# Kernel optimization log

Measured on AMD Instinct MI355X. Metric: run time of the kernel, lower is better.

The kernel has to match this reference:

```python
import jax, jax.numpy as jnp
import numpy as np

N_HEADS, D_MODEL, D_HEAD = 16, 1024, 64
INIT_RANGE = 0.02
BATCH, SEQ = 4, 2048


def setup_inputs() -> dict:
    key = jax.random.key(0)
    k0, k1, k2, k3, k4 = jax.random.split(key, 5)
    resid = jax.random.normal(k0, (BATCH, SEQ, D_MODEL), dtype=jnp.float32)
    w_q = INIT_RANGE * jax.random.normal(k1, (N_HEADS, D_MODEL, D_HEAD), dtype=jnp.float32)
    w_k = INIT_RANGE * jax.random.normal(k2, (N_HEADS, D_MODEL, D_HEAD), dtype=jnp.float32)
    w_v = INIT_RANGE * jax.random.normal(k3, (N_HEADS, D_MODEL, D_HEAD), dtype=jnp.float32)
    w_o = INIT_RANGE * jax.random.normal(k4, (N_HEADS, D_HEAD, D_MODEL), dtype=jnp.float32)
    return {"resid": resid, "w_q": w_q, "w_k": w_k, "w_v": w_v, "w_o": w_o}


def reference(resid, w_q, w_k, w_v, w_o):
    # resid: [b, s, m]; w_q/k/v: [h, m, d]; w_o: [h, d, m]
    qs = jnp.einsum('bsm,hmd->bhsd', resid, w_q)
    ks = jnp.einsum('bsm,hmd->bhsd', resid, w_k)
    vs = jnp.einsum('bsm,hmd->bhsd', resid, w_v)
    attn = jnp.einsum('bhqd,bhkd->bhqk', qs, ks)  # full O(n^2) scores
    s = attn.shape[-1]
    causal = jnp.tril(jnp.ones((s, s), dtype=bool))  # True = keep
    attn = jnp.where(causal, attn, -jnp.inf)
    attn = jax.nn.softmax(attn / jnp.sqrt(jnp.float32(D_HEAD)), axis=-1)
    z = jnp.einsum('bhqk,bhkd->bhqd', attn, vs)
    out = jnp.einsum('bhsd,hdm->bsm', z, w_o)
    return out
```

## Files before the change

### kernel.cpp

```cpp
#include <hip/hip_runtime.h>


typedef __attribute__((ext_vector_type(8))) short short8;
typedef __attribute__((ext_vector_type(4))) float f32x4;
typedef __attribute__((ext_vector_type(16))) float f32x16;

#define GLDS16(g, l) __builtin_amdgcn_global_load_lds(                        \
    (const __attribute__((address_space(1))) unsigned int*)(g),               \
    (__attribute__((address_space(3))) unsigned int*)(l), 16, 0, 0)

static __device__ __forceinline__ unsigned short f2b(float f) {
  union { float f; unsigned u; } c; c.f = f;
  unsigned r = c.u + 0x7fffu + ((c.u >> 16) & 1u);
  return (unsigned short)(r >> 16);
}

__global__ void k_cast(const float* __restrict__ x, unsigned short* __restrict__ o, int n4) {
  int i = blockIdx.x * blockDim.x + threadIdx.x;
  if (i >= n4) return;
  float4 v = reinterpret_cast<const float4*>(x)[i];
  ushort4 u;
  u.x = f2b(v.x); u.y = f2b(v.y); u.z = f2b(v.z); u.w = f2b(v.w);
  reinterpret_cast<ushort4*>(o)[i] = u;
}

__global__ void k_trans_qkv(const float* __restrict__ wq, const float* __restrict__ wk,
                            const float* __restrict__ wv, unsigned short* __restrict__ o) {
  __shared__ float t[64][65];
  int blk = blockIdx.x;
  int mt = blk & 15;
  int h = (blk >> 4) & 15;
  int which = blk >> 8;
  const float* w = which == 0 ? wq : (which == 1 ? wk : wv);
  int tid = threadIdx.x;
  int m0 = mt * 64;
  #pragma unroll
  for (int rep = 0; rep < 16; ++rep) {
    int idx = rep * 256 + tid;
    int r = idx >> 6, c = idx & 63;
    t[r][c] = w[(h * 1024 + m0 + r) * 64 + c];
  }
  __syncthreads();
  #pragma unroll
  for (int rep = 0; rep < 16; ++rep) {
    int idx = rep * 256 + tid;
    int dr = idx >> 6, mc = idx & 63;
    o[(which * 1024 + h * 64 + dr) * 1024 + m0 + mc] = f2b(t[mc][dr]);
  }
}

__global__ void k_trans_wo(const float* __restrict__ wo, unsigned short* __restrict__ o) {
  __shared__ float t[64][65];
  int blk = blockIdx.x;
  int mt = blk & 15, kt = blk >> 4;
  int tid = threadIdx.x;
  int k0 = kt * 64, m0 = mt * 64;
  #pragma unroll
  for (int rep = 0; rep < 16; ++rep) {
    int idx = rep * 256 + tid;
    int r = idx >> 6, c = idx & 63;
    t[r][c] = wo[(k0 + r) * 1024 + m0 + c];
  }
  __syncthreads();
  #pragma unroll
  for (int rep = 0; rep < 16; ++rep) {
    int idx = rep * 256 + tid;
    int r = idx >> 6, c = idx & 63;
    o[(m0 + r) * 1024 + k0 + c] = f2b(t[c][r]);
  }
}

__global__ __launch_bounds__(256) void k_gemm_qkv(const unsigned short* __restrict__ A,
                                                  const unsigned short* __restrict__ Bt,
                                                  unsigned short* __restrict__ Qb,
                                                  unsigned short* __restrict__ Kc,
                                                  unsigned short* __restrict__ Vc) {
  __shared__ unsigned short As[128 * 32];
  __shared__ unsigned short Bs[128 * 32];
  const int bm = blockIdx.x, bn = blockIdx.y;
  const int tid = threadIdx.x;
  const int lane = tid & 63, wid = tid >> 6;
  const int wr = wid >> 1, wc = wid & 1;
  const int fr = lane & 15, fq = lane >> 4;
  const int which = bn >> 3;

  f32x4 acc[4][4];
  #pragma unroll
  for (int i = 0; i < 4; ++i)
    #pragma unroll
    for (int n = 0; n < 4; ++n) acc[i][n] = f32x4{0.f, 0.f, 0.f, 0.f};

  const int arow = tid >> 2, acol = (tid & 3) * 8;
  const int lds0 = tid * 8, lds1 = (tid + 256) * 8;
  const unsigned short* aG0 = A + (bm * 128 + arow) * 1024 + acol;
  const unsigned short* aG1 = A + (bm * 128 + arow + 64) * 1024 + acol;
  const unsigned short* bG0 = Bt + (bn * 128 + arow) * 1024 + acol;
  const unsigned short* bG1 = Bt + (bn * 128 + arow + 64) * 1024 + acol;

  const unsigned short* Ar = As + (wr * 64 + fr) * 32 + fq * 8;
  const unsigned short* Br = Bs + (wc * 64 + fr) * 32 + fq * 8;

  if (which == 2) {
    for (int k0 = 0; k0 < 1024; k0 += 32) {
      __syncthreads();
      GLDS16(aG0 + k0, As + lds0);
      GLDS16(aG1 + k0, As + lds1);
      GLDS16(bG0 + k0, Bs + lds0);
      GLDS16(bG1 + k0, Bs + lds1);
      asm volatile("s_waitcnt vmcnt(0)" ::: "memory");
      __syncthreads();
      short8 a[4], b[4];
      #pragma unroll
      for (int i = 0; i < 4; ++i) a[i] = *reinterpret_cast<const short8*>(Ar + i * 512);
      #pragma unroll
      for (int n = 0; n < 4; ++n) b[n] = *reinterpret_cast<const short8*>(Br + n * 512);
      #pragma unroll
      for (int i = 0; i < 4; ++i)
        #pragma unroll
        for (int n = 0; n < 4; ++n)
          acc[i][n] = __builtin_amdgcn_mfma_f32_16x16x32_bf16(a[i], b[n], acc[i][n], 0, 0, 0);
    }
    const int colb = bn * 128 + wc * 64 + fr - 2048;
    const int rowb = bm * 128 + wr * 64 + fq * 4;
    #pragma unroll
    for (int n = 0; n < 4; ++n) {
      const int rc = colb + n * 16;
      const int h = rc >> 6, d = rc & 63;
      #pragma unroll
      for (int i = 0; i < 4; ++i) {
        const int row = rowb + i * 16;
        const int b_ = row >> 11, s = row & 2047;
        const int bh = b_ * 16 + h;
        const int c = s >> 5, kk = s & 31;
        const int r = d >> 1;
        const int sl = (((d & 1) * 4 + (kk >> 3)) ^ (r & 7));
        ushort4 v;
        v.x = f2b(acc[i][n][0]); v.y = f2b(acc[i][n][1]);
        v.z = f2b(acc[i][n][2]); v.w = f2b(acc[i][n][3]);
        *reinterpret_cast<ushort4*>(
            &Vc[((size_t)(bh * 64 + c)) * 2048 + r * 64 + sl * 8 + (kk & 7)]) = v;
      }
    }
  } else {
    for (int k0 = 0; k0 < 1024; k0 += 32) {
      __syncthreads();
      GLDS16(aG0 + k0, As + lds0);
      GLDS16(aG1 + k0, As + lds1);
      GLDS16(bG0 + k0, Bs + lds0);
      GLDS16(bG1 + k0, Bs + lds1);
      asm volatile("s_waitcnt vmcnt(0)" ::: "memory");
      __syncthreads();
      short8 a[4], b[4];
      #pragma unroll
      for (int i = 0; i < 4; ++i) a[i] = *reinterpret_cast<const short8*>(Ar + i * 512);
      #pragma unroll
      for (int n = 0; n < 4; ++n) b[n] = *reinterpret_cast<const short8*>(Br + n * 512);
      #pragma unroll
      for (int i = 0; i < 4; ++i)
        #pragma unroll
        for (int n = 0; n < 4; ++n)
          acc[i][n] = __builtin_amdgcn_mfma_f32_16x16x32_bf16(b[n], a[i], acc[i][n], 0, 0, 0);
    }
    const float CS = 0.125f * 1.44269504088896340736f;
    const int rowS = bm * 128 + wr * 64 + fr;
    const int cold = bn * 128 + wc * 64 + fq * 4;
    #pragma unroll
    for (int i = 0; i < 4; ++i) {
      const int S = rowS + i * 16;
      const int b_ = S >> 11, s = S & 2047;
      #pragma unroll
      for (int n = 0; n < 4; ++n) {
        const int col = cold + n * 16;
        const int rc = col & 1023;
        const int h = rc >> 6, d0 = rc & 63;
        const int bh = b_ * 16 + h;
        if (which == 0) {
          ushort4 u;
          u.x = f2b(acc[i][n][0] * CS); u.y = f2b(acc[i][n][1] * CS);
          u.z = f2b(acc[i][n][2] * CS); u.w = f2b(acc[i][n][3] * CS);
          *reinterpret_cast<ushort4*>(&Qb[((size_t)bh * 2048 + s) * 64 + d0]) = u;
        } else {
          const int c = s >> 5, r = s & 31;
          const int dsw0 = (((d0 >> 3) ^ (r & 7)) << 3) | (d0 & 7);
          ushort4 u;
          u.x = f2b(acc[i][n][0]); u.y = f2b(acc[i][n][1]);
          u.z = f2b(acc[i][n][2]); u.w = f2b(acc[i][n][3]);
          *reinterpret_cast<ushort4*>(
              &Kc[(((size_t)(bh * 64 + c)) * 32 + r) * 64 + dsw0]) = u;
        }
      }
    }
  }
}


static __device__ __forceinline__ f32x16 mfma32(short8 a, short8 b, f32x16 c) {
  return __builtin_amdgcn_mfma_f32_32x32x16_bf16(a, b, c, 0, 0, 0);
}

template<bool MASKED>
static __device__ __forceinline__ void compute_chunk(
    const unsigned short* __restrict__ Kl, const unsigned short* __restrict__ Vl,
    int q, int hi,
    const short8& Qf0, const short8& Qf1, const short8& Qf2, const short8& Qf3,
    f32x16& accA, f32x16& accB, float& lsum) {
  const int qs = q & 7;
  const short8 kf0 = *reinterpret_cast<const short8*>(Kl + q * 64 + (((0 + hi) ^ qs) << 3));
  const short8 kf1 = *reinterpret_cast<const short8*>(Kl + q * 64 + (((2 + hi) ^ qs) << 3));
  const short8 kf2 = *reinterpret_cast<const short8*>(Kl + q * 64 + (((4 + hi) ^ qs) << 3));
  const short8 kf3 = *reinterpret_cast<const short8*>(Kl + q * 64 + (((6 + hi) ^ qs) << 3));
  const int vr = q >> 1, vs = (q & 1) * 4, vw = vr & 7;
  const short8 v00 = *reinterpret_cast<const short8*>(Vl + vr * 64 + (((vs + hi) ^ vw) << 3));
  const short8 v01 = *reinterpret_cast<const short8*>(Vl + vr * 64 + (((vs + 2 + hi) ^ vw) << 3));
  const short8 v10 = *reinterpret_cast<const short8*>(Vl + (vr + 16) * 64 + (((vs + hi) ^ vw) << 3));
  const short8 v11 = *reinterpret_cast<const short8*>(Vl + (vr + 16) * 64 + (((vs + 2 + hi) ^ vw) << 3));

  f32x16 s = {0.f,0.f,0.f,0.f,0.f,0.f,0.f,0.f,0.f,0.f,0.f,0.f,0.f,0.f,0.f,0.f};
  s = mfma32(kf0, Qf0, s);
  s = mfma32(kf1, Qf1, s);
  s = mfma32(kf2, Qf2, s);
  s = mfma32(kf3, Qf3, s);

  float p[16];
  #pragma unroll
  for (int r = 0; r < 16; ++r) {
    if (MASKED) {
      const int kr = (r & 3) + 8 * (r >> 2) + 4 * hi;
      p[r] = (kr <= q) ? __builtin_amdgcn_exp2f(s[r]) : 0.f;
    } else {
      p[r] = __builtin_amdgcn_exp2f(s[r]);
    }
  }
  float t0 = (p[0] + p[1]) + (p[2] + p[3]);
  float t1 = (p[4] + p[5]) + (p[6] + p[7]);
  float t2 = (p[8] + p[9]) + (p[10] + p[11]);
  float t3 = (p[12] + p[13]) + (p[14] + p[15]);
  lsum += (t0 + t1) + (t2 + t3);

  unsigned W[8], X[8];
  #pragma unroll
  for (int i = 0; i < 8; ++i)
    asm("v_cvt_pk_bf16_f32 %0, %1, %2" : "=v"(W[i]) : "v"(p[2 * i]), "v"(p[2 * i + 1]));
  #pragma unroll
  for (int i = 0; i < 8; ++i) X[i] = __shfl_xor(W[i], 32);

  union { unsigned u[4]; short8 v; } fa0, fa1;
  fa0.u[0] = hi ? X[2] : W[0];
  fa0.u[1] = hi ? X[3] : W[1];
  fa0.u[2] = hi ? W[2] : X[0];
  fa0.u[3] = hi ? W[3] : X[1];
  fa1.u[0] = hi ? X[6] : W[4];
  fa1.u[1] = hi ? X[7] : W[5];
  fa1.u[2] = hi ? W[6] : X[4];
  fa1.u[3] = hi ? W[7] : X[5];

  accA = mfma32(fa0.v, v00, accA);
  accA = mfma32(fa1.v, v01, accA);
  accB = mfma32(fa0.v, v10, accB);
  accB = mfma32(fa1.v, v11, accB);
}

static __device__ __forceinline__ void store_tile(unsigned short* __restrict__ Zb,
    int b_, int h, int q0, int q, int hi,
    const f32x16& a0, const f32x16& a1, float lsum) {
  const float lt = lsum + __shfl_xor(lsum, 32);
  const float rl = 1.f / lt;
  #pragma unroll
  for (int r = 0; r < 16; ++r) {
    const int qr = (r & 3) + 8 * (r >> 2) + 4 * hi;
    const float rlr = __shfl(rl, qr);
    unsigned short* dst = Zb + ((size_t)(b_ * 2048 + q0 + qr)) * 1024 + h * 64 + q;
    dst[0]  = f2b(a0[r] * rlr);
    dst[32] = f2b(a1[r] * rlr);
  }
}

__global__ __launch_bounds__(256, 2) void k_attn(const unsigned short* __restrict__ Qb,
                                                 const unsigned short* __restrict__ Kc,
                                                 const unsigned short* __restrict__ Vc,
                                                 unsigned short* __restrict__ Zb) {
  __shared__ __align__(16) unsigned short Kbuf[2][2048];
  __shared__ __align__(16) unsigned short Vbuf[2][2048];
  const int tid = threadIdx.x;
  const int lane = tid & 63, w = tid >> 6;
  const int q = lane & 31, hi = lane >> 5;
  const int bid = blockIdx.x;
  const int bh = (bid & 7) * 8 + ((bid >> 3) & 7);
  const int P1 = bid >> 6;
  const int b_ = bh >> 4, h = bh & 15;

  const unsigned short* Qbh = Qb + (size_t)bh * 2048 * 64;
  const unsigned short* Kch = Kc + (size_t)bh * 64 * 2048;
  const unsigned short* Vch = Vc + (size_t)bh * 64 * 2048;

  #pragma unroll 1
  for (int t = 0; t < 2; ++t) {
    const int P = t ? (15 - P1) : P1;
    const int q0 = 128 * P + 32 * w;
    const int cmax = 4 * P + w;
    const int C = 4 * P + 4;

    const unsigned short* Qp = Qbh + (size_t)(q0 + q) * 64 + hi * 8;
    const short8 Qf0 = *reinterpret_cast<const short8*>(Qp);
    const short8 Qf1 = *reinterpret_cast<const short8*>(Qp + 16);
    const short8 Qf2 = *reinterpret_cast<const short8*>(Qp + 32);
    const short8 Qf3 = *reinterpret_cast<const short8*>(Qp + 48);

    f32x16 a0 = {0.f,0.f,0.f,0.f,0.f,0.f,0.f,0.f,0.f,0.f,0.f,0.f,0.f,0.f,0.f,0.f};
    f32x16 a1 = a0;
    float l = 0.f;

    GLDS16(Kch + tid * 8, &Kbuf[0][tid * 8]);
    GLDS16(Vch + tid * 8, &Vbuf[0][tid * 8]);

    for (int c = 0; c < C; ++c) {
      if (c + 1 < C) {
        const int par = (c + 1) & 1;
        GLDS16(Kch + (size_t)(c + 1) * 2048 + tid * 8, &Kbuf[par][tid * 8]);
        GLDS16(Vch + (size_t)(c + 1) * 2048 + tid * 8, &Vbuf[par][tid * 8]);
        asm volatile("s_waitcnt vmcnt(2)" ::: "memory");
      } else {
        asm volatile("s_waitcnt vmcnt(0)" ::: "memory");
      }
      __syncthreads();
      if (c <= cmax) {
        const int par = c & 1;
        if (c == cmax)
          compute_chunk<true>(Kbuf[par], Vbuf[par], q, hi, Qf0, Qf1, Qf2, Qf3, a0, a1, l);
        else
          compute_chunk<false>(Kbuf[par], Vbuf[par], q, hi, Qf0, Qf1, Qf2, Qf3, a0, a1, l);
      }
      __syncthreads();
    }
    store_tile(Zb, b_, h, q0, q, hi, a0, a1, l);
  }
}

__global__ __launch_bounds__(256) void k_gemm_out(const unsigned short* __restrict__ A,
                                                  const unsigned short* __restrict__ Bt,
                                                  float* __restrict__ Out) {
  __shared__ unsigned short As[128 * 32];
  __shared__ unsigned short Bs[128 * 32];
  const int bm = blockIdx.x, bn = blockIdx.y;
  const int tid = threadIdx.x;
  const int lane = tid & 63, wid = tid >> 6;
  const int wr = wid >> 1, wc = wid & 1;
  const int fr = lane & 15, fq = lane >> 4;

  f32x4 acc[4][4];
  #pragma unroll
  for (int i = 0; i < 4; ++i)
    #pragma unroll
    for (int n = 0; n < 4; ++n) acc[i][n] = f32x4{0.f, 0.f, 0.f, 0.f};

  const int arow = tid >> 2, acol = (tid & 3) * 8;
  const int lds0 = tid * 8, lds1 = (tid + 256) * 8;
  const unsigned short* aG0 = A + (bm * 128 + arow) * 1024 + acol;
  const unsigned short* aG1 = A + (bm * 128 + arow + 64) * 1024 + acol;
  const unsigned short* bG0 = Bt + (bn * 128 + arow) * 1024 + acol;
  const unsigned short* bG1 = Bt + (bn * 128 + arow + 64) * 1024 + acol;

  const unsigned short* Ar = As + (wr * 64 + fr) * 32 + fq * 8;
  const unsigned short* Br = Bs + (wc * 64 + fr) * 32 + fq * 8;

  for (int k0 = 0; k0 < 1024; k0 += 32) {
    __syncthreads();
    GLDS16(aG0 + k0, As + lds0);
    GLDS16(aG1 + k0, As + lds1);
    GLDS16(bG0 + k0, Bs + lds0);
    GLDS16(bG1 + k0, Bs + lds1);
    asm volatile("s_waitcnt vmcnt(0)" ::: "memory");
    __syncthreads();
    short8 a[4], b[4];
    #pragma unroll
    for (int i = 0; i < 4; ++i) a[i] = *reinterpret_cast<const short8*>(Ar + i * 512);
    #pragma unroll
    for (int n = 0; n < 4; ++n) b[n] = *reinterpret_cast<const short8*>(Br + n * 512);
    #pragma unroll
    for (int i = 0; i < 4; ++i)
      #pragma unroll
      for (int n = 0; n < 4; ++n)
        acc[i][n] = __builtin_amdgcn_mfma_f32_16x16x32_bf16(b[n], a[i], acc[i][n], 0, 0, 0);
  }

  const int rowS = bm * 128 + wr * 64 + fr;
  const int cold = bn * 128 + wc * 64 + fq * 4;
  #pragma unroll
  for (int i = 0; i < 4; ++i) {
    const int S = rowS + i * 16;
    #pragma unroll
    for (int n = 0; n < 4; ++n) {
      const int m0 = cold + n * 16;
      float4 v;
      v.x = acc[i][n][0]; v.y = acc[i][n][1]; v.z = acc[i][n][2]; v.w = acc[i][n][3];
      *reinterpret_cast<float4*>(&Out[(size_t)S * 1024 + m0]) = v;
    }
  }
}

extern "C" void kernel_launch(void* const* d_in, const int* in_sizes, int n_in,
                              void* d_out, int out_size, void* d_ws, size_t ws_size,
                              hipStream_t stream) {
  const float* resid = (const float*)d_in[0];
  const float* w_q = (const float*)d_in[1];
  const float* w_k = (const float*)d_in[2];
  const float* w_v = (const float*)d_in[3];
  const float* w_o = (const float*)d_in[4];
  float* out = (float*)d_out;

  char* ws = (char*)d_ws;
  const size_t MB = 1u << 20;
  unsigned short* Xb = (unsigned short*)(ws);
  unsigned short* W3 = (unsigned short*)(ws + 16 * MB);
  unsigned short* Wo = (unsigned short*)(ws + 22 * MB);
  unsigned short* Qb = (unsigned short*)(ws + 24 * MB);
  unsigned short* Kc = (unsigned short*)(ws + 40 * MB);
  unsigned short* Vc = (unsigned short*)(ws + 56 * MB);
  unsigned short* Zb = Xb;

  hipLaunchKernelGGL(k_cast, dim3(8192), dim3(256), 0, stream, resid, Xb, 8192 * 1024 / 4);
  hipLaunchKernelGGL(k_trans_qkv, dim3(768), dim3(256), 0, stream, w_q, w_k, w_v, W3);
  hipLaunchKernelGGL(k_trans_wo, dim3(256), dim3(256), 0, stream, w_o, Wo);
  hipLaunchKernelGGL(k_gemm_qkv, dim3(64, 24), dim3(256), 0, stream, Xb, W3, Qb, Kc, Vc);
  hipLaunchKernelGGL(k_attn, dim3(512), dim3(256), 0, stream, Qb, Kc, Vc, Zb);
  hipLaunchKernelGGL(k_gemm_out, dim3(64, 8), dim3(256), 0, stream, Zb, Wo, out);
}
```

Before: 189.3 us.

## Double-buffer GEMM LDS tiles and pre-swizzle bf16 operands against bank conflicts

The QKV and output-projection GEMMs now double-buffer their LDS tiles, so the global-to-LDS load of the next K slice is issued before the MFMAs on the current one. This drops one barrier per iteration and overlaps memory with compute. All bf16 operand producers (the cast, the weight transposes and the attention output store) now write a swizzled layout within each 32-column group. The GEMMs read LDS with the matching XOR slot, which avoids LDS bank conflicts without changing the direct global_load_lds copy. LDS per block doubles, which may reduce occupancy, and every producer and consumer must agree on the swizzle.

```diff
diff --git a/kernel.cpp b/kernel.cpp
--- a/kernel.cpp
+++ b/kernel.cpp
@@ -13,6 +13,10 @@
   union { float f; unsigned u; } c; c.f = f;
   unsigned r = c.u + 0x7fffu + ((c.u >> 16) & 1u);
   return (unsigned short)(r >> 16);
+}
+
+static __device__ __forceinline__ int swzc(int row, int c) {
+  return (c & ~31) | ((((c >> 3) & 3) ^ ((row >> 1) & 3)) << 3) | (c & 7);
 }
 
 __global__ void k_cast(const float* __restrict__ x, unsigned short* __restrict__ o, int n4) {
@@ -21,7 +25,9 @@
   float4 v = reinterpret_cast<const float4*>(x)[i];
   ushort4 u;
   u.x = f2b(v.x); u.y = f2b(v.y); u.z = f2b(v.z); u.w = f2b(v.w);
-  reinterpret_cast<ushort4*>(o)[i] = u;
+  const int flat = i * 4;
+  const int row = flat >> 10, c = flat & 1023;
+  *reinterpret_cast<ushort4*>(&o[row * 1024 + swzc(row, c)]) = u;
 }
 
 __global__ void k_trans_qkv(const float* __restrict__ wq, const float* __restrict__ wk,
@@ -45,7 +51,8 @@
   for (int rep = 0; rep < 16; ++rep) {
     int idx = rep * 256 + tid;
     int dr = idx >> 6, mc = idx & 63;
-    o[(which * 1024 + h * 64 + dr) * 1024 + m0 + mc] = f2b(t[mc][dr]);
+    const int row = which * 1024 + h * 64 + dr;
+    o[row * 1024 + swzc(dr, m0 + mc)] = f2b(t[mc][dr]);
   }
 }
 
@@ -66,7 +73,7 @@
   for (int rep = 0; rep < 16; ++rep) {
     int idx = rep * 256 + tid;
     int r = idx >> 6, c = idx & 63;
-    o[(m0 + r) * 1024 + k0 + c] = f2b(t[c][r]);
+    o[(m0 + r) * 1024 + swzc(r, k0 + c)] = f2b(t[c][r]);
   }
 }
 
@@ -75,8 +82,8 @@
                                                   unsigned short* __restrict__ Qb,
                                                   unsigned short* __restrict__ Kc,
                                                   unsigned short* __restrict__ Vc) {
-  __shared__ unsigned short As[128 * 32];
-  __shared__ unsigned short Bs[128 * 32];
+  __shared__ unsigned short As[2][128 * 32];
+  __shared__ unsigned short Bs[2][128 * 32];
   const int bm = blockIdx.x, bn = blockIdx.y;
   const int tid = threadIdx.x;
   const int lane = tid & 63, wid = tid >> 6;
@@ -91,35 +98,56 @@
     for (int n = 0; n < 4; ++n) acc[i][n] = f32x4{0.f, 0.f, 0.f, 0.f};
 
   const int arow = tid >> 2, acol = (tid & 3) * 8;
-  const int lds0 = tid * 8, lds1 = (tid + 256) * 8;
+  const int lds0 = tid * 8, lds1 = tid * 8 + 2048;
   const unsigned short* aG0 = A + (bm * 128 + arow) * 1024 + acol;
   const unsigned short* aG1 = A + (bm * 128 + arow + 64) * 1024 + acol;
   const unsigned short* bG0 = Bt + (bn * 128 + arow) * 1024 + acol;
   const unsigned short* bG1 = Bt + (bn * 128 + arow + 64) * 1024 + acol;
 
-  const unsigned short* Ar = As + (wr * 64 + fr) * 32 + fq * 8;
-  const unsigned short* Br = Bs + (wc * 64 + fr) * 32 + fq * 8;
-
-  if (which == 2) {
-    for (int k0 = 0; k0 < 1024; k0 += 32) {
-      __syncthreads();
-      GLDS16(aG0 + k0, As + lds0);
-      GLDS16(aG1 + k0, As + lds1);
-      GLDS16(bG0 + k0, Bs + lds0);
-      GLDS16(bG1 + k0, Bs + lds1);
-      asm volatile("s_waitcnt vmcnt(0)" ::: "memory");
-      __syncthreads();
-      short8 a[4], b[4];
-      #pragma unroll
-      for (int i = 0; i < 4; ++i) a[i] = *reinterpret_cast<const short8*>(Ar + i * 512);
-      #pragma unroll
-      for (int n = 0; n < 4; ++n) b[n] = *reinterpret_cast<const short8*>(Br + n * 512);
+  const int rowA = (wr * 64 + fr) * 32;
+  const int rowB = (wc * 64 + fr) * 32;
+  const int slot = ((fq ^ ((fr >> 1) & 3)) << 3);
+
+  GLDS16(aG0, As[0] + lds0);
+  GLDS16(aG1, As[0] + lds1);
+  GLDS16(bG0, Bs[0] + lds0);
+  GLDS16(bG1, Bs[0] + lds1);
+  asm volatile("s_waitcnt vmcnt(0)" ::: "memory");
+  __syncthreads();
+
+  for (int k0 = 0; k0 < 1024; k0 += 32) {
+    const int cur = (k0 >> 5) & 1;
+    if (k0 + 32 < 1024) {
+      GLDS16(aG0 + k0 + 32, As[cur ^ 1] + lds0);
+      GLDS16(aG1 + k0 + 32, As[cur ^ 1] + lds1);
+      GLDS16(bG0 + k0 + 32, Bs[cur ^ 1] + lds0);
+      GLDS16(bG1 + k0 + 32, Bs[cur ^ 1] + lds1);
+    }
+    short8 a[4], b[4];
+    #pragma unroll
+    for (int i = 0; i < 4; ++i)
+      a[i] = *reinterpret_cast<const short8*>(As[cur] + rowA + i * 512 + slot);
+    #pragma unroll
+    for (int n = 0; n < 4; ++n)
+      b[n] = *reinterpret_cast<const short8*>(Bs[cur] + rowB + n * 512 + slot);
+    if (which == 2) {
       #pragma unroll
       for (int i = 0; i < 4; ++i)
         #pragma unroll
         for (int n = 0; n < 4; ++n)
           acc[i][n] = __builtin_amdgcn_mfma_f32_16x16x32_bf16(a[i], b[n], acc[i][n], 0, 0, 0);
-    }
+    } else {
+      #pragma unroll
+      for (int i = 0; i < 4; ++i)
+        #pragma unroll
+        for (int n = 0; n < 4; ++n)
+          acc[i][n] = __builtin_amdgcn_mfma_f32_16x16x32_bf16(b[n], a[i], acc[i][n], 0, 0, 0);
+    }
+    asm volatile("s_waitcnt vmcnt(0)" ::: "memory");
+    __syncthreads();
+  }
+
+  if (which == 2) {
     const int colb = bn * 128 + wc * 64 + fr - 2048;
     const int rowb = bm * 128 + wr * 64 + fq * 4;
     #pragma unroll
@@ -142,25 +170,6 @@
       }
     }
   } else {
-    for (int k0 = 0; k0 < 1024; k0 += 32) {
-      __syncthreads();
-      GLDS16(aG0 + k0, As + lds0);
-      GLDS16(aG1 + k0, As + lds1);
-      GLDS16(bG0 + k0, Bs + lds0);
-      GLDS16(bG1 + k0, Bs + lds1);
-      asm volatile("s_waitcnt vmcnt(0)" ::: "memory");
-      __syncthreads();
-      short8 a[4], b[4];
-      #pragma unroll
-      for (int i = 0; i < 4; ++i) a[i] = *reinterpret_cast<const short8*>(Ar + i * 512);
-      #pragma unroll
-      for (int n = 0; n < 4; ++n) b[n] = *reinterpret_cast<const short8*>(Br + n * 512);
-      #pragma unroll
-      for (int i = 0; i < 4; ++i)
-        #pragma unroll
-        for (int n = 0; n < 4; ++n)
-          acc[i][n] = __builtin_amdgcn_mfma_f32_16x16x32_bf16(b[n], a[i], acc[i][n], 0, 0, 0);
-    }
     const float CS = 0.125f * 1.44269504088896340736f;
     const int rowS = bm * 128 + wr * 64 + fr;
     const int cold = bn * 128 + wc * 64 + fq * 4;
@@ -269,9 +278,11 @@
   for (int r = 0; r < 16; ++r) {
     const int qr = (r & 3) + 8 * (r >> 2) + 4 * hi;
     const float rlr = __shfl(rl, qr);
-    unsigned short* dst = Zb + ((size_t)(b_ * 2048 + q0 + qr)) * 1024 + h * 64 + q;
-    dst[0]  = f2b(a0[r] * rlr);
-    dst[32] = f2b(a1[r] * rlr);
+    const int row = b_ * 2048 + q0 + qr;
+    const int sl = (((q >> 3) ^ ((qr >> 1) & 3)) << 3) + (q & 7);
+    unsigned short* dst = Zb + (size_t)row * 1024 + h * 64;
+    dst[sl]      = f2b(a0[r] * rlr);
+    dst[32 + sl] = f2b(a1[r] * rlr);
   }
 }
 
@@ -339,8 +350,8 @@
 __global__ __launch_bounds__(256) void k_gemm_out(const unsigned short* __restrict__ A,
                                                   const unsigned short* __restrict__ Bt,
                                                   float* __restrict__ Out) {
-  __shared__ unsigned short As[128 * 32];
-  __shared__ unsigned short Bs[128 * 32];
+  __shared__ unsigned short As[2][128 * 32];
+  __shared__ unsigned short Bs[2][128 * 32];
   const int bm = blockIdx.x, bn = blockIdx.y;
   const int tid = threadIdx.x;
   const int lane = tid & 63, wid = tid >> 6;
@@ -354,33 +365,45 @@
     for (int n = 0; n < 4; ++n) acc[i][n] = f32x4{0.f, 0.f, 0.f, 0.f};
 
   const int arow = tid >> 2, acol = (tid & 3) * 8;
-  const int lds0 = tid * 8, lds1 = (tid + 256) * 8;
+  const int lds0 = tid * 8, lds1 = tid * 8 + 2048;
   const unsigned short* aG0 = A + (bm * 128 + arow) * 1024 + acol;
   const unsigned short* aG1 = A + (bm * 128 + arow + 64) * 1024 + acol;
   const unsigned short* bG0 = Bt + (bn * 128 + arow) * 1024 + acol;
   const unsigned short* bG1 = Bt + (bn * 128 + arow + 64) * 1024 + acol;
 
-  const unsigned short* Ar = As + (wr * 64 + fr) * 32 + fq * 8;
-  const unsigned short* Br = Bs + (wc * 64 + fr) * 32 + fq * 8;
+  const int rowA = (wr * 64 + fr) * 32;
+  const int rowB = (wc * 64 + fr) * 32;
+  const int slot = ((fq ^ ((fr >> 1) & 3)) << 3);
+
+  GLDS16(aG0, As[0] + lds0);
+  GLDS16(aG1, As[0] + lds1);
+  GLDS16(bG0, Bs[0] + lds0);
+  GLDS16(bG1, Bs[0] + lds1);
+  asm volatile("s_waitcnt vmcnt(0)" ::: "memory");
+  __syncthreads();
 
   for (int k0 = 0; k0 < 1024; k0 += 32) {
-    __syncthreads();
-    GLDS16(aG0 + k0, As + lds0);
-    GLDS16(aG1 + k0, As + lds1);
-    GLDS16(bG0 + k0, Bs + lds0);
-    GLDS16(bG1 + k0, Bs + lds1);
-    asm volatile("s_waitcnt vmcnt(0)" ::: "memory");
-    __syncthreads();
+    const int cur = (k0 >> 5) & 1;
+    if (k0 + 32 < 1024) {
+      GLDS16(aG0 + k0 + 32, As[cur ^ 1] + lds0);
+      GLDS16(aG1 + k0 + 32, As[cur ^ 1] + lds1);
+      GLDS16(bG0 + k0 + 32, Bs[cur ^ 1] + lds0);
+      GLDS16(bG1 + k0 + 32, Bs[cur ^ 1] + lds1);
+    }
     short8 a[4], b[4];
     #pragma unroll
-    for (int i = 0; i < 4; ++i) a[i] = *reinterpret_cast<const short8*>(Ar + i * 512);
-    #pragma unroll
-    for (int n = 0; n < 4; ++n) b[n] = *reinterpret_cast<const short8*>(Br + n * 512);
+    for (int i = 0; i < 4; ++i)
+      a[i] = *reinterpret_cast<const short8*>(As[cur] + rowA + i * 512 + slot);
+    #pragma unroll
+    for (int n = 0; n < 4; ++n)
+      b[n] = *reinterpret_cast<const short8*>(Bs[cur] + rowB + n * 512 + slot);
     #pragma unroll
     for (int i = 0; i < 4; ++i)
       #pragma unroll
       for (int n = 0; n < 4; ++n)
         acc[i][n] = __builtin_amdgcn_mfma_f32_16x16x32_bf16(b[n], a[i], acc[i][n], 0, 0, 0);
+    asm volatile("s_waitcnt vmcnt(0)" ::: "memory");
+    __syncthreads();
   }
 
   const int rowS = bm * 128 + wr * 64 + fr;
```

Result: slower. 197.4 us (+4.3%).
